# Kernel tuning notes

Hardware: AMD Instinct MI355X
Metric: run time of the kernel (lower is better)

Reference implementation:

```python
import jax, jax.numpy as jnp
import numpy as np

B, S, H = 2, 2048, 1024
NH = 16
HD = H // NH
MLP = 32


def setup_inputs() -> dict:
    key = jax.random.key(0)
    ks = jax.random.split(key, 24)
    def lin(k, fan_in, shape):
        bound = 1.0 / np.sqrt(fan_in)
        return jax.random.uniform(k, shape, jnp.float32, -bound, bound)
    return {
        "hidden_states": jax.random.normal(ks[0], (B, S, H), jnp.float32),
        "importance_scores": jax.random.uniform(ks[1], (B, S), jnp.float32),
        "wq": lin(ks[2], H, (H, H)), "bq": lin(ks[3], H, (H,)),
        "wk": lin(ks[4], H, (H, H)), "bk": lin(ks[5], H, (H,)),
        "wv": lin(ks[6], H, (H, H)), "bv": lin(ks[7], H, (H,)),
        "wo": lin(ks[8], H, (H, H)), "bo": lin(ks[9], H, (H,)),
        "rw1": lin(ks[10], 1, (1, MLP)), "rb1": lin(ks[11], 1, (MLP,)),
        "rw2": lin(ks[12], MLP, (MLP, NH)), "rb2": lin(ks[13], MLP, (NH,)),
        "aw1": lin(ks[14], 1, (1, MLP)), "ab1": lin(ks[15], 1, (MLP,)),
        "aw2": lin(ks[16], MLP, (MLP, NH)), "ab2": lin(ks[17], MLP, (NH,)),
        "log_temperature": jnp.zeros((NH,), jnp.float32),
        "ln_g": jnp.ones((H,), jnp.float32),
        "ln_b": jnp.zeros((H,), jnp.float32),
    }


def _forward(hidden_states, importance_scores, wq, bq, wk, bk, wv, bv, wo, bo,
             rw1, rb1, rw2, rb2, aw1, ab1, aw2, ab2, log_temperature, ln_g, ln_b):
    Bs, Ss, Hs = hidden_states.shape
    # Q, K, V: (B, NH, S, HD)
    def proj(w, b):
        return (hidden_states @ w + b).reshape(Bs, Ss, NH, HD).transpose(0, 2, 1, 3)
    Q, K, V = proj(wq, bq), proj(wk, bk), proj(wv, bv)
    scale = jnp.sqrt(jnp.float32(HD))
    attn_logits = jnp.einsum('bhqd,bhkd->bhqk', Q, K) / scale

    imp = importance_scores[..., None]  # (B, S, 1)
    def mlp(w1, b1, w2, b2):
        h = jax.nn.gelu(imp @ w1 + b1, approximate=False)
        return h @ w2 + b2  # (B, S, NH)
    reach = mlp(rw1, rb1, rw2, rb2).transpose(0, 2, 1)[..., None]      # (B,NH,S,1)
    attract = mlp(aw1, ab1, aw2, ab2).transpose(0, 2, 1)[..., None, :]  # (B,NH,1,S)

    pos = jnp.arange(Ss, dtype=jnp.float32)
    dist = jnp.abs(pos[None, :] - pos[:, None])  # (S, S); matches |i-j| (symmetric)
    temperature = jnp.exp(log_temperature).reshape(1, NH, 1, 1) + 1.0
    normalized_dist = dist[None, None] / Ss
    mask_logits = reach + attract - normalized_dist / temperature
    mask_bias = jnp.log(jax.nn.sigmoid(mask_logits) + 1e-8)

    attn_weights = jax.nn.softmax(attn_logits + mask_bias, axis=-1)
    attn_out = jnp.einsum('bhqk,bhkd->bhqd', attn_weights, V)
    attn_out = attn_out.transpose(0, 2, 1, 3).reshape(Bs, Ss, Hs)
    out = attn_out @ wo + bo

    x = hidden_states + out
    mu = jnp.mean(x, axis=-1, keepdims=True)
    var = jnp.mean(jnp.square(x - mu), axis=-1, keepdims=True)
    return (x - mu) / jnp.sqrt(var + 1e-5) * ln_g + ln_b


def reference(hidden_states, importance_scores, wq, bq, wk, bk, wv, bv, wo, bo,
              rw1, rb1, rw2, rb2, aw1, ab1, aw2, ab2, log_temperature, ln_g, ln_b):
    return _forward(hidden_states, importance_scores, wq, bq, wk, bk, wv, bv, wo, bo,
                    rw1, rb1, rw2, rb2, aw1, ab1, aw2, ab2, log_temperature, ln_g, ln_b)
```

## Files before the change

### kernel.cpp

```cpp
#include <hip/hip_runtime.h>
#include <math.h>

#define NB 2
#define NS 2048
#define NHID 1024
#define NHEAD 16
#define DHEAD 64

typedef _Float16 half_t;
typedef _Float16 hx4 __attribute__((ext_vector_type(4)));
typedef _Float16 hx8 __attribute__((ext_vector_type(8)));
typedef float fx4 __attribute__((ext_vector_type(4)));

typedef const __attribute__((address_space(1))) void* gvp;
typedef __attribute__((address_space(3))) void* svp;

static __device__ __forceinline__ void gload16(const void* g, void* s) {
  __builtin_amdgcn_global_load_lds((gvp)g, (svp)s, 16, 0, 0);
}

static __device__ __forceinline__ float gelu_exact(float x) {
  return 0.5f * x * (1.0f + erff(x * 0.70710678118654752f));
}

__launch_bounds__(256)
__global__ void packx(const float* __restrict__ x, half_t* __restrict__ xb) {
  const int i = blockIdx.x * 256 + threadIdx.x;
  const fx4 v = ((const fx4*)x)[i];
  hx4 o;
#pragma unroll
  for (int j = 0; j < 4; ++j) o[j] = (half_t)v[j];
  ((hx4*)xb)[i] = o;
}

__launch_bounds__(256)
__global__ void packw(const float* __restrict__ w0, const float* __restrict__ w1,
                      const float* __restrict__ w2, const float* __restrict__ w3,
                      half_t* __restrict__ o0, half_t* __restrict__ o1,
                      half_t* __restrict__ o2, half_t* __restrict__ o3) {
  __shared__ float tile[32][33];
  const int z = blockIdx.z;
  const float* w = (z == 0) ? w0 : (z == 1) ? w1 : (z == 2) ? w2 : w3;
  half_t* o = (z == 0) ? o0 : (z == 1) ? o1 : (z == 2) ? o2 : o3;
  const int n0 = blockIdx.x * 32, k0 = blockIdx.y * 32;
  const int tx = threadIdx.x, ty = threadIdx.y;
#pragma unroll
  for (int i = 0; i < 4; ++i)
    tile[ty + i * 8][tx] = w[(size_t)(k0 + ty + i * 8) * NHID + n0 + tx];
  __syncthreads();
#pragma unroll
  for (int i = 0; i < 4; ++i)
    o[(size_t)(n0 + ty + i * 8) * NHID + k0 + tx] = (half_t)tile[tx][ty + i * 8];
}

__launch_bounds__(256)
__global__ void mlp16(const float* __restrict__ imp,
                      const float* __restrict__ rw1, const float* __restrict__ rb1,
                      const float* __restrict__ rw2, const float* __restrict__ rb2,
                      const float* __restrict__ aw1, const float* __restrict__ ab1,
                      const float* __restrict__ aw2, const float* __restrict__ ab2,
                      float* __restrict__ reach, float* __restrict__ attract) {
  const int i = blockIdx.x * 256 + threadIdx.x;
  const float v = imp[i];
  const int b = i >> 11, s = i & (NS - 1);
  float ra[16] = {}, aa[16] = {};
  for (int m = 0; m < 32; ++m) {
    const float hr = gelu_exact(v * rw1[m] + rb1[m]);
    const float ha = gelu_exact(v * aw1[m] + ab1[m]);
#pragma unroll
    for (int h = 0; h < 16; ++h) {
      ra[h] += hr * rw2[m * 16 + h];
      aa[h] += ha * aw2[m * 16 + h];
    }
  }
#pragma unroll
  for (int h = 0; h < 16; ++h) {
    reach[(size_t)(b * NHEAD + h) * NS + s] = ra[h] + rb2[h];
    attract[(size_t)(b * NHEAD + h) * NS + s] = aa[h] + ab2[h];
  }
}

__launch_bounds__(256, 2)
__global__ void gemm_qkv(const half_t* __restrict__ A,
                         const half_t* __restrict__ Wq, const half_t* __restrict__ Wk,
                         const half_t* __restrict__ Wv,
                         const float* __restrict__ bq, const float* __restrict__ bk,
                         const float* __restrict__ bv,
                         half_t* __restrict__ Qo, half_t* __restrict__ Ko,
                         half_t* __restrict__ Vo) {
  __shared__ __align__(16) half_t As[128 * 32];
  __shared__ __align__(16) half_t Bs[128 * 32];
  const int z = blockIdx.z;
  const half_t* Bt = (z == 0) ? Wq : (z == 1) ? Wk : Wv;
  const float* bias = (z == 0) ? bq : (z == 1) ? bk : bv;

  const int t = threadIdx.x;
  const int l = t & 63, w = t >> 6;
  const int lo = l & 15, g = l >> 4;
  const int m0 = blockIdx.x * 128, n0 = blockIdx.y * 128;
  const int wm = (w >> 1) * 64, wn = (w & 1) * 64;
  fx4 acc[4][4] = {};

  for (int k0 = 0; k0 < NHID; k0 += 32) {
#pragma unroll
    for (int i = 0; i < 2; ++i) {
      const int c = i * 256 + t;
      const int row = c >> 2, kc = (c & 3) * 8;
      gload16(A + (size_t)(m0 + row) * NHID + k0 + kc, As + c * 8);
      gload16(Bt + (size_t)(n0 + row) * NHID + k0 + kc, Bs + c * 8);
    }
    __syncthreads();
    hx8 af[4], bfv[4];
#pragma unroll
    for (int i = 0; i < 4; ++i) {
      af[i] = *(const hx8*)(As + (wm + i * 16 + lo) * 32 + g * 8);
      bfv[i] = *(const hx8*)(Bs + (wn + i * 16 + lo) * 32 + g * 8);
    }
#pragma unroll
    for (int mi = 0; mi < 4; ++mi)
#pragma unroll
      for (int ni = 0; ni < 4; ++ni)
        acc[mi][ni] = __builtin_amdgcn_mfma_f32_16x16x32_f16(af[mi], bfv[ni], acc[mi][ni], 0, 0, 0);
    __syncthreads();
  }

#pragma unroll
  for (int mi = 0; mi < 4; ++mi) {
    const int r0 = m0 + wm + mi * 16 + g * 4;
#pragma unroll
    for (int ni = 0; ni < 4; ++ni) {
      const int col = n0 + wn + ni * 16 + lo;
      const float bs = bias[col];
      if (z == 2) {
        const int b = r0 >> 11, s = r0 & (NS - 1);
        const int h = col >> 6, d = col & 63;
        hx4 v;
#pragma unroll
        for (int j = 0; j < 4; ++j) v[j] = (half_t)(acc[mi][ni][j] + bs);
        *(hx4*)(Vo + ((size_t)((b * NHEAD + h) * DHEAD + d)) * NS + s) = v;
      } else if (z == 0) {
#pragma unroll
        for (int j = 0; j < 4; ++j)
          Qo[(size_t)(r0 + j) * NHID + col] = (half_t)((acc[mi][ni][j] + bs) * 0.125f);
      } else {
#pragma unroll
        for (int j = 0; j < 4; ++j)
          Ko[(size_t)(r0 + j) * NHID + col] = (half_t)(acc[mi][ni][j] + bs);
      }
    }
  }
}

__launch_bounds__(256, 2)
__global__ void gemm_o(const half_t* __restrict__ A, const half_t* __restrict__ Bt,
                       const float* __restrict__ bias, const float* __restrict__ resid,
                       float* __restrict__ outf) {
  __shared__ __align__(16) half_t As[128 * 32];
  __shared__ __align__(16) half_t Bs[128 * 32];
  const int t = threadIdx.x;
  const int l = t & 63, w = t >> 6;
  const int lo = l & 15, g = l >> 4;
  const int m0 = blockIdx.x * 128, n0 = blockIdx.y * 128;
  const int wm = (w >> 1) * 64, wn = (w & 1) * 64;
  fx4 acc[4][4] = {};

  for (int k0 = 0; k0 < NHID; k0 += 32) {
#pragma unroll
    for (int i = 0; i < 2; ++i) {
      const int c = i * 256 + t;
      const int row = c >> 2, kc = (c & 3) * 8;
      gload16(A + (size_t)(m0 + row) * NHID + k0 + kc, As + c * 8);
      gload16(Bt + (size_t)(n0 + row) * NHID + k0 + kc, Bs + c * 8);
    }
    __syncthreads();
    hx8 af[4], bfv[4];
#pragma unroll
    for (int i = 0; i < 4; ++i) {
      af[i] = *(const hx8*)(As + (wm + i * 16 + lo) * 32 + g * 8);
      bfv[i] = *(const hx8*)(Bs + (wn + i * 16 + lo) * 32 + g * 8);
    }
#pragma unroll
    for (int mi = 0; mi < 4; ++mi)
#pragma unroll
      for (int ni = 0; ni < 4; ++ni)
        acc[mi][ni] = __builtin_amdgcn_mfma_f32_16x16x32_f16(af[mi], bfv[ni], acc[mi][ni], 0, 0, 0);
    __syncthreads();
  }

#pragma unroll
  for (int mi = 0; mi < 4; ++mi) {
    const int r0 = m0 + wm + mi * 16 + g * 4;
#pragma unroll
    for (int ni = 0; ni < 4; ++ni) {
      const int col = n0 + wn + ni * 16 + lo;
      const float bs = bias[col];
#pragma unroll
      for (int j = 0; j < 4; ++j) {
        const size_t idx = (size_t)(r0 + j) * NHID + col;
        outf[idx] = acc[mi][ni][j] + bs + resid[idx];
      }
    }
  }
}

__launch_bounds__(256, 2)
__global__ void attn64(const half_t* __restrict__ Qb, const half_t* __restrict__ Kb,
                       const half_t* __restrict__ Vtb,
                       const float* __restrict__ reach, const float* __restrict__ attract,
                       const float* __restrict__ ltemp,
                       half_t* __restrict__ O) {
  __shared__ __align__(16) half_t Ks[64 * 64];
  __shared__ __align__(16) half_t Vs[64 * 64];
  __shared__ __align__(16) half_t Ps[4][16 * 80];
  __shared__ float attS[64];

  const int t = threadIdx.x;
  const int l = t & 63, w = t >> 6;
  const int lo = l & 15, g = l >> 4;
  const int bh = blockIdx.y;
  const int b = bh >> 4, h = bh & 15;
  const int q0 = blockIdx.x * 64;
  const int q = q0 + w * 16 + lo;

  const float invtemp = 1.0f / (__expf(ltemp[h]) + 1.0f);
  const float ndc = invtemp * (1.0f / (float)NS);
  const float rq = reach[(size_t)bh * NS + q];

  hx8 qf[2];
  {
    const half_t* qp = Qb + (size_t)(b * NS + q) * NHID + h * DHEAD + g * 8;
    qf[0] = *(const hx8*)(qp);
    qf[1] = *(const hx8*)(qp + 32);
  }

  fx4 o[4] = {};
  float m_run = -INFINITY, s_run = 0.0f;

  const half_t* Kbase = Kb + (size_t)b * (NS * NHID) + h * DHEAD;
  const half_t* Vbase = Vtb + (size_t)bh * (DHEAD * NS);
  const float* abase = attract + (size_t)bh * NS;

  for (int kv0 = 0; kv0 < NS; kv0 += 64) {
#pragma unroll
    for (int i = 0; i < 2; ++i) {
      const int c = i * 256 + t;
      const int row = c >> 3;
      const int ca = (c & 7) ^ (row & 7);
      gload16(Kbase + (size_t)(kv0 + row) * NHID + ca * 8, Ks + c * 8);
      gload16(Vbase + (size_t)row * NS + kv0 + ca * 8, Vs + c * 8);
    }
    if (t < 64) attS[t] = abase[kv0 + t];
    __syncthreads();

    fx4 sa[4] = {};
#pragma unroll
    for (int mf = 0; mf < 4; ++mf) {
      const int row = mf * 16 + lo;
#pragma unroll
      for (int ks = 0; ks < 2; ++ks) {
        const hx8 kf = *(const hx8*)(Ks + row * 64 + (((ks * 4 + g) ^ (row & 7)) * 8));
        sa[mf] = __builtin_amdgcn_mfma_f32_16x16x32_f16(kf, qf[ks], sa[mf], 0, 0, 0);
      }
    }

    float tmax = -INFINITY;
#pragma unroll
    for (int mf = 0; mf < 4; ++mf)
#pragma unroll
      for (int j = 0; j < 4; ++j) tmax = fmaxf(tmax, sa[mf][j]);
    tmax = fmaxf(tmax, __shfl_xor(tmax, 16));
    tmax = fmaxf(tmax, __shfl_xor(tmax, 32));
    const float m_new = fmaxf(m_run, tmax);
    const float alpha = __expf(m_run - m_new);

    float psum = 0.0f;
    hx4 pb[4];
#pragma unroll
    for (int mf = 0; mf < 4; ++mf) {
#pragma unroll
      for (int j = 0; j < 4; ++j) {
        const int kvl = mf * 16 + g * 4 + j;
        const float x = rq + attS[kvl] - fabsf((float)(q - (kv0 + kvl))) * ndc;
        const float e = __expf(sa[mf][j] - m_new);
        const float sg = 1.0f / (1.0f + __expf(-x));
        const float p = e * (sg + 1e-8f);
        psum += p;
        pb[mf][j] = (half_t)p;
      }
    }
    psum += __shfl_xor(psum, 16);
    psum += __shfl_xor(psum, 32);
    s_run = s_run * alpha + psum;
    m_run = m_new;
#pragma unroll
    for (int df = 0; df < 4; ++df) {
#pragma unroll
      for (int j = 0; j < 4; ++j) o[df][j] *= alpha;
    }
#pragma unroll
    for (int mf = 0; mf < 4; ++mf)
      *(hx4*)(&Ps[w][lo * 80 + mf * 16 + g * 4]) = pb[mf];

#pragma unroll
    for (int df = 0; df < 4; ++df) {
      const int row = df * 16 + lo;
#pragma unroll
      for (int ks = 0; ks < 2; ++ks) {
        const hx8 vf = *(const hx8*)(Vs + row * 64 + (((ks * 4 + g) ^ (row & 7)) * 8));
        const hx8 pf = *(const hx8*)(&Ps[w][lo * 80 + ks * 32 + g * 8]);
        o[df] = __builtin_amdgcn_mfma_f32_16x16x32_f16(vf, pf, o[df], 0, 0, 0);
      }
    }
    __syncthreads();
  }

  const float inv = 1.0f / s_run;
  half_t* ob = O + (size_t)(b * NS + q) * NHID + h * DHEAD + g * 4;
#pragma unroll
  for (int df = 0; df < 4; ++df) {
    hx4 v;
#pragma unroll
    for (int j = 0; j < 4; ++j) v[j] = (half_t)(o[df][j] * inv);
    *(hx4*)(ob + df * 16) = v;
  }
}

__launch_bounds__(256)
__global__ void lnorm(const float* __restrict__ y, const float* __restrict__ g,
                      const float* __restrict__ bta, float* __restrict__ out) {
  const int row = blockIdx.x;
  const int t = threadIdx.x;
  const fx4 v = ((const fx4*)(y + (size_t)row * NHID))[t];
  float s = v[0] + v[1] + v[2] + v[3];
  float sq = v[0] * v[0] + v[1] * v[1] + v[2] * v[2] + v[3] * v[3];
#pragma unroll
  for (int off = 1; off < 64; off <<= 1) {
    s += __shfl_xor(s, off);
    sq += __shfl_xor(sq, off);
  }
  __shared__ float rs[4], rsq[4];
  const int w = t >> 6;
  if ((t & 63) == 0) { rs[w] = s; rsq[w] = sq; }
  __syncthreads();
  s = rs[0] + rs[1] + rs[2] + rs[3];
  sq = rsq[0] + rsq[1] + rsq[2] + rsq[3];
  const float mu = s * (1.0f / NHID);
  const float var = sq * (1.0f / NHID) - mu * mu;
  const float rstd = rsqrtf(fmaxf(var, 0.0f) + 1e-5f);
  const fx4 gg = ((const fx4*)g)[t];
  const fx4 bb = ((const fx4*)bta)[t];
  fx4 o;
#pragma unroll
  for (int j = 0; j < 4; ++j) o[j] = (v[j] - mu) * rstd * gg[j] + bb[j];
  ((fx4*)(out + (size_t)row * NHID))[t] = o;
}

extern "C" void kernel_launch(void* const* d_in, const int* in_sizes, int n_in,
                              void* d_out, int out_size, void* d_ws, size_t ws_size,
                              hipStream_t stream) {
  const float* hidden = (const float*)d_in[0];
  const float* imp = (const float*)d_in[1];
  const float* wq = (const float*)d_in[2];  const float* bq = (const float*)d_in[3];
  const float* wk = (const float*)d_in[4];  const float* bk = (const float*)d_in[5];
  const float* wv = (const float*)d_in[6];  const float* bv = (const float*)d_in[7];
  const float* wo = (const float*)d_in[8];  const float* bo = (const float*)d_in[9];
  const float* rw1 = (const float*)d_in[10]; const float* rb1 = (const float*)d_in[11];
  const float* rw2 = (const float*)d_in[12]; const float* rb2 = (const float*)d_in[13];
  const float* aw1 = (const float*)d_in[14]; const float* ab1 = (const float*)d_in[15];
  const float* aw2 = (const float*)d_in[16]; const float* ab2 = (const float*)d_in[17];
  const float* ltemp = (const float*)d_in[18];
  const float* lng = (const float*)d_in[19]; const float* lnb = (const float*)d_in[20];

  char* ws = (char*)d_ws;
  half_t* Xb  = (half_t*)(ws);
  half_t* Wqt = (half_t*)(ws + (size_t)(8u << 20));
  half_t* Wkt = (half_t*)(ws + (size_t)(10u << 20));
  half_t* Wvt = (half_t*)(ws + (size_t)(12u << 20));
  half_t* Wot = (half_t*)(ws + (size_t)(14u << 20));
  half_t* Qb  = (half_t*)(ws + (size_t)(16u << 20));
  half_t* Kb  = (half_t*)(ws + (size_t)(24u << 20));
  half_t* Vtb = (half_t*)(ws + (size_t)(32u << 20));
  half_t* AO  = (half_t*)(ws + (size_t)(40u << 20));
  float*  reach   = (float*)(ws + (size_t)(48u << 20));
  float*  attract = (float*)(ws + (size_t)(48u << 20) + 262144);
  float*  Y = (float*)(ws + (size_t)(16u << 20));

  packx<<<dim3(4096), dim3(256), 0, stream>>>(hidden, Xb);
  packw<<<dim3(32, 32, 4), dim3(32, 8), 0, stream>>>(wq, wk, wv, wo, Wqt, Wkt, Wvt, Wot);
  mlp16<<<dim3(16), dim3(256), 0, stream>>>(imp, rw1, rb1, rw2, rb2, aw1, ab1, aw2, ab2,
                                            reach, attract);
  gemm_qkv<<<dim3(32, 8, 3), dim3(256), 0, stream>>>(Xb, Wqt, Wkt, Wvt, bq, bk, bv,
                                                     Qb, Kb, Vtb);
  attn64<<<dim3(32, 32), dim3(256), 0, stream>>>(Qb, Kb, Vtb, reach, attract, ltemp, AO);
  gemm_o<<<dim3(32, 8), dim3(256), 0, stream>>>(AO, Wot, bo, hidden, Y);
  lnorm<<<dim3(4096), dim3(256), 0, stream>>>(Y, lng, lnb, (float*)d_out);
}
```

Before: 332.0 us.

## Double-buffer attention KV tiles, use exp2 softmax with lazy rescale, split V transpose

Attention now prefetches the next K/V tile into a second LDS buffer while computing on the current one. The softmax and sigmoid move to the exp2 domain by folding log2(e) into the Q scale, reach and attract, and the distance term is precomputed as per-key min/max offsets. Rescaling of the running max is skipped unless it grows by more than a threshold, and P feeds the 16x16x16 MFMA directly from registers, which removes the LDS round trip for P. The V transpose leaves the QKV GEMM epilogue and becomes a separate tiled transpose kernel, so all three projections write coalesced rows, at the cost of one extra launch and an extra pass over V. Occupancy hints rise to four blocks per CU.

```diff
diff --git a/kernel.cpp b/kernel.cpp
--- a/kernel.cpp
+++ b/kernel.cpp
@@ -11,6 +11,9 @@
 typedef _Float16 hx4 __attribute__((ext_vector_type(4)));
 typedef _Float16 hx8 __attribute__((ext_vector_type(8)));
 typedef float fx4 __attribute__((ext_vector_type(4)));
+
+#define RLN2 1.4426950408889634f
+#define SCALE_Q 0.18033688011112042f
 
 typedef const __attribute__((address_space(1))) void* gvp;
 typedef __attribute__((address_space(3))) void* svp;
@@ -75,8 +78,8 @@
   }
 #pragma unroll
   for (int h = 0; h < 16; ++h) {
-    reach[(size_t)(b * NHEAD + h) * NS + s] = ra[h] + rb2[h];
-    attract[(size_t)(b * NHEAD + h) * NS + s] = aa[h] + ab2[h];
+    reach[(size_t)(b * NHEAD + h) * NS + s] = (ra[h] + rb2[h]) * RLN2;
+    attract[(size_t)(b * NHEAD + h) * NS + s] = (aa[h] + ab2[h]) * RLN2;
   }
 }
 
@@ -93,6 +96,8 @@
   const int z = blockIdx.z;
   const half_t* Bt = (z == 0) ? Wq : (z == 1) ? Wk : Wv;
   const float* bias = (z == 0) ? bq : (z == 1) ? bk : bv;
+  half_t* Co = (z == 0) ? Qo : (z == 1) ? Ko : Vo;
+  const float oscale = (z == 0) ? SCALE_Q : 1.0f;
 
   const int t = threadIdx.x;
   const int l = t & 63, w = t >> 6;
@@ -131,23 +136,31 @@
     for (int ni = 0; ni < 4; ++ni) {
       const int col = n0 + wn + ni * 16 + lo;
       const float bs = bias[col];
-      if (z == 2) {
-        const int b = r0 >> 11, s = r0 & (NS - 1);
-        const int h = col >> 6, d = col & 63;
-        hx4 v;
-#pragma unroll
-        for (int j = 0; j < 4; ++j) v[j] = (half_t)(acc[mi][ni][j] + bs);
-        *(hx4*)(Vo + ((size_t)((b * NHEAD + h) * DHEAD + d)) * NS + s) = v;
-      } else if (z == 0) {
-#pragma unroll
-        for (int j = 0; j < 4; ++j)
-          Qo[(size_t)(r0 + j) * NHID + col] = (half_t)((acc[mi][ni][j] + bs) * 0.125f);
-      } else {
-#pragma unroll
-        for (int j = 0; j < 4; ++j)
-          Ko[(size_t)(r0 + j) * NHID + col] = (half_t)(acc[mi][ni][j] + bs);
-      }
-    }
+#pragma unroll
+      for (int j = 0; j < 4; ++j)
+        Co[(size_t)(r0 + j) * NHID + col] = (half_t)((acc[mi][ni][j] + bs) * oscale);
+    }
+  }
+}
+
+__launch_bounds__(256)
+__global__ void vtrans(const half_t* __restrict__ in, half_t* __restrict__ out) {
+  __shared__ half_t tile[64][72];
+  const int b = blockIdx.z, s0 = blockIdx.x * 64, n0 = blockIdx.y * 64;
+  const int t = threadIdx.x;
+  const int r = t >> 3, c = (t & 7) * 8;
+  const half_t* ip = in + ((size_t)(b * NS) + s0) * NHID + n0;
+#pragma unroll
+  for (int i = 0; i < 2; ++i)
+    *(hx8*)&tile[r + i * 32][c] = *(const hx8*)(ip + (size_t)(r + i * 32) * NHID + c);
+  __syncthreads();
+  half_t* op = out + ((size_t)(b * NHID) + n0) * NS + s0;
+#pragma unroll
+  for (int i = 0; i < 2; ++i) {
+    hx8 v;
+#pragma unroll
+    for (int j = 0; j < 8; ++j) v[j] = tile[c + j][r + i * 32];
+    *(hx8*)(op + (size_t)(r + i * 32) * NS + c) = v;
   }
 }
 
@@ -203,16 +216,15 @@
   }
 }
 
-__launch_bounds__(256, 2)
+__launch_bounds__(256, 4)
 __global__ void attn64(const half_t* __restrict__ Qb, const half_t* __restrict__ Kb,
                        const half_t* __restrict__ Vtb,
                        const float* __restrict__ reach, const float* __restrict__ attract,
                        const float* __restrict__ ltemp,
                        half_t* __restrict__ O) {
-  __shared__ __align__(16) half_t Ks[64 * 64];
-  __shared__ __align__(16) half_t Vs[64 * 64];
-  __shared__ __align__(16) half_t Ps[4][16 * 80];
-  __shared__ float attS[64];
+  __shared__ __align__(16) half_t Ks[2][64 * 64];
+  __shared__ __align__(16) half_t Vs[2][64 * 64];
+  __shared__ float apS[2][64], amS[2][64];
 
   const int t = threadIdx.x;
   const int l = t & 63, w = t >> 6;
@@ -222,9 +234,10 @@
   const int q0 = blockIdx.x * 64;
   const int q = q0 + w * 16 + lo;
 
-  const float invtemp = 1.0f / (__expf(ltemp[h]) + 1.0f);
-  const float ndc = invtemp * (1.0f / (float)NS);
+  const float ndc2 = RLN2 / ((__expf(ltemp[h]) + 1.0f) * (float)NS);
   const float rq = reach[(size_t)bh * NS + q];
+  const float cqm = rq - (float)q * ndc2;
+  const float cqp = rq + (float)q * ndc2;
 
   hx8 qf[2];
   {
@@ -240,75 +253,107 @@
   const half_t* Vbase = Vtb + (size_t)bh * (DHEAD * NS);
   const float* abase = attract + (size_t)bh * NS;
 
-  for (int kv0 = 0; kv0 < NS; kv0 += 64) {
-#pragma unroll
-    for (int i = 0; i < 2; ++i) {
-      const int c = i * 256 + t;
-      const int row = c >> 3;
-      const int ca = (c & 7) ^ (row & 7);
-      gload16(Kbase + (size_t)(kv0 + row) * NHID + ca * 8, Ks + c * 8);
-      gload16(Vbase + (size_t)row * NS + kv0 + ca * 8, Vs + c * 8);
-    }
-    if (t < 64) attS[t] = abase[kv0 + t];
-    __syncthreads();
+#pragma unroll
+  for (int i = 0; i < 2; ++i) {
+    const int c = i * 256 + t;
+    const int row = c >> 3;
+    const int ca = (c & 7) ^ (row & 7);
+    gload16(Kbase + (size_t)row * NHID + ca * 8, &Ks[0][c * 8]);
+    gload16(Vbase + (size_t)row * NS + ca * 8, &Vs[0][c * 8]);
+  }
+  if (t < 64) {
+    const float a = abase[t];
+    apS[0][t] = a + (float)t * ndc2;
+    amS[0][t] = a - (float)t * ndc2;
+  }
+  __syncthreads();
+
+  int buf = 0;
+  for (int kv0 = 0; kv0 < NS; kv0 += 64, buf ^= 1) {
+    if (kv0 + 64 < NS) {
+      const int nb = buf ^ 1;
+      const int kvn = kv0 + 64;
+#pragma unroll
+      for (int i = 0; i < 2; ++i) {
+        const int c = i * 256 + t;
+        const int row = c >> 3;
+        const int ca = (c & 7) ^ (row & 7);
+        gload16(Kbase + (size_t)(kvn + row) * NHID + ca * 8, &Ks[nb][c * 8]);
+        gload16(Vbase + (size_t)row * NS + kvn + ca * 8, &Vs[nb][c * 8]);
+      }
+      if (t < 64) {
+        const float a = abase[kvn + t];
+        const float kvf = (float)(kvn + t);
+        apS[nb][t] = a + kvf * ndc2;
+        amS[nb][t] = a - kvf * ndc2;
+      }
+    }
 
     fx4 sa[4] = {};
 #pragma unroll
     for (int mf = 0; mf < 4; ++mf) {
       const int row = mf * 16 + lo;
+      const half_t* kr = &Ks[buf][row * 64];
+      const int rx = row & 7;
 #pragma unroll
       for (int ks = 0; ks < 2; ++ks) {
-        const hx8 kf = *(const hx8*)(Ks + row * 64 + (((ks * 4 + g) ^ (row & 7)) * 8));
+        const hx8 kf = *(const hx8*)(kr + (((ks * 4 + g) ^ rx) * 8));
         sa[mf] = __builtin_amdgcn_mfma_f32_16x16x32_f16(kf, qf[ks], sa[mf], 0, 0, 0);
       }
     }
 
-    float tmax = -INFINITY;
+    float tmax = -1e30f;
 #pragma unroll
     for (int mf = 0; mf < 4; ++mf)
 #pragma unroll
       for (int j = 0; j < 4; ++j) tmax = fmaxf(tmax, sa[mf][j]);
     tmax = fmaxf(tmax, __shfl_xor(tmax, 16));
     tmax = fmaxf(tmax, __shfl_xor(tmax, 32));
-    const float m_new = fmaxf(m_run, tmax);
-    const float alpha = __expf(m_run - m_new);
+    if (!__all(tmax - m_run <= 10.0f)) {
+      const float m_new = fmaxf(m_run, tmax);
+      const float al = __builtin_amdgcn_exp2f(m_run - m_new);
+      s_run *= al;
+#pragma unroll
+      for (int df = 0; df < 4; ++df)
+#pragma unroll
+        for (int j = 0; j < 4; ++j) o[df][j] *= al;
+      m_run = m_new;
+    }
 
     float psum = 0.0f;
     hx4 pb[4];
 #pragma unroll
     for (int mf = 0; mf < 4; ++mf) {
+      const fx4 ap = *(const fx4*)&apS[buf][mf * 16 + g * 4];
+      const fx4 am = *(const fx4*)&amS[buf][mf * 16 + g * 4];
+      float pe[4];
 #pragma unroll
       for (int j = 0; j < 4; ++j) {
-        const int kvl = mf * 16 + g * 4 + j;
-        const float x = rq + attS[kvl] - fabsf((float)(q - (kv0 + kvl))) * ndc;
-        const float e = __expf(sa[mf][j] - m_new);
-        const float sg = 1.0f / (1.0f + __expf(-x));
-        const float p = e * (sg + 1e-8f);
+        const float x = fminf(cqm + ap[j], cqp + am[j]);
+        const float e = __builtin_amdgcn_exp2f(sa[mf][j] - m_run);
+        const float u = __builtin_amdgcn_exp2f(-x);
+        const float p = e * __builtin_amdgcn_rcpf(1.0f + u);
         psum += p;
-        pb[mf][j] = (half_t)p;
-      }
+        pe[j] = p;
+      }
+      const auto c0 = __builtin_amdgcn_cvt_pkrtz(pe[0], pe[1]);
+      const auto c1 = __builtin_amdgcn_cvt_pkrtz(pe[2], pe[3]);
+      pb[mf][0] = (half_t)c0[0]; pb[mf][1] = (half_t)c0[1];
+      pb[mf][2] = (half_t)c1[0]; pb[mf][3] = (half_t)c1[1];
     }
     psum += __shfl_xor(psum, 16);
     psum += __shfl_xor(psum, 32);
-    s_run = s_run * alpha + psum;
-    m_run = m_new;
+    s_run += psum;
+
 #pragma unroll
     for (int df = 0; df < 4; ++df) {
-#pragma unroll
-      for (int j = 0; j < 4; ++j) o[df][j] *= alpha;
-    }
-#pragma unroll
-    for (int mf = 0; mf < 4; ++mf)
-      *(hx4*)(&Ps[w][lo * 80 + mf * 16 + g * 4]) = pb[mf];
-
-#pragma unroll
-    for (int df = 0; df < 4; ++df) {
-      const int row = df * 16 + lo;
-#pragma unroll
-      for (int ks = 0; ks < 2; ++ks) {
-        const hx8 vf = *(const hx8*)(Vs + row * 64 + (((ks * 4 + g) ^ (row & 7)) * 8));
-        const hx8 pf = *(const hx8*)(&Ps[w][lo * 80 + ks * 32 + g * 8]);
-        o[df] = __builtin_amdgcn_mfma_f32_16x16x32_f16(vf, pf, o[df], 0, 0, 0);
+      const int r = df * 16 + lo;
+      const half_t* vr = &Vs[buf][r * 64 + (g & 1) * 4];
+      const int rx = r & 7;
+#pragma unroll
+      for (int mf = 0; mf < 4; ++mf) {
+        const hx4 vf = *(const hx4*)(vr + (((2 * mf + (g >> 1)) ^ rx) * 8));
+        o[df] = __builtin_amdgcn_mfma_f32_16x16x16f16(vf, pb[mf], o[df], 0, 0, 0);
       }
     }
     __syncthreads();
@@ -380,6 +425,7 @@
   half_t* Qb  = (half_t*)(ws + (size_t)(16u << 20));
   half_t* Kb  = (half_t*)(ws + (size_t)(24u << 20));
   half_t* Vtb = (half_t*)(ws + (size_t)(32u << 20));
+  half_t* Vb  = (half_t*)(ws + (size_t)(40u << 20));
   half_t* AO  = (half_t*)(ws + (size_t)(40u << 20));
   float*  reach   = (float*)(ws + (size_t)(48u << 20));
   float*  attract = (float*)(ws + (size_t)(48u << 20) + 262144);
@@ -390,7 +436,8 @@
   mlp16<<<dim3(16), dim3(256), 0, stream>>>(imp, rw1, rb1, rw2, rb2, aw1, ab1, aw2, ab2,
                                             reach, attract);
   gemm_qkv<<<dim3(32, 8, 3), dim3(256), 0, stream>>>(Xb, Wqt, Wkt, Wvt, bq, bk, bv,
-                                                     Qb, Kb, Vtb);
+                                                     Qb, Kb, Vb);
+  vtrans<<<dim3(32, 16, 2), dim3(256), 0, stream>>>(Vb, Vtb);
   attn64<<<dim3(32, 32), dim3(256), 0, stream>>>(Qb, Kb, Vtb, reach, attract, ltemp, AO);
   gemm_o<<<dim3(32, 8), dim3(256), 0, stream>>>(AO, Wot, bo, hidden, Y);
   lnorm<<<dim3(4096), dim3(256), 0, stream>>>(Y, lng, lnb, (float*)d_out);
```

New measurement: 288.3 us. -13.1%, faster.
